# Performance work log

Hardware: AMD Instinct MI355X
Metric: run time of the kernel (lower is better)

## Reference

```python
import jax, jax.numpy as jnp
import numpy as np

B, T = 16, 2048
OBS_DIM, ACT_DIM, HIDDEN = 64, 16, 512


def setup_inputs() -> dict:
    key = jax.random.key(0)
    ks = jax.random.split(key, 6)
    n = lambda k, shape, scale: (jax.random.normal(k, shape, dtype=jnp.float32) * scale)
    return {
        "obs": n(ks[0], (B, T, OBS_DIM), 1.0),
        "act": n(ks[1], (B, T, ACT_DIM), 1.0),
        "W_e": n(ks[2], (HIDDEN, OBS_DIM + ACT_DIM), 0.05),   # embed Linear weight
        "b_e": jnp.zeros((HIDDEN,), jnp.float32),             # embed Linear bias
        "a_raw": n(ks[3], (HIDDEN,), 0.5),                    # diagonal decay (pre-tanh)
        "W_B": n(ks[4], (HIDDEN, HIDDEN), 0.02),              # B Linear weight (no bias)
        "W_out": n(ks[5], (OBS_DIM, HIDDEN), 0.04),           # out Linear weight
        "b_out": jnp.zeros((OBS_DIM,), jnp.float32),          # out Linear bias
    }


def reference(obs, act, W_e, b_e, a_raw, W_B, W_out, b_out):
    # x: [B, T, obs+act]
    x = jnp.concatenate([obs, act], axis=-1)
    # embed: Linear + ReLU, batched over all timesteps -> u: [B, T, H]
    u = jax.nn.relu(jnp.einsum('btd,hd->bth', x, W_e) + b_e)
    # B projection batched over all t (the per-step matmul in the torch loop)
    v = jnp.einsum('bth,gh->btg', u, W_B)  # [B, T, H]
    a = jnp.tanh(a_raw)  # [H]
    # Diagonal linear recurrence s_t = a * s_{t-1} + v_t, s_0 starting from zeros,
    # realized as a parallel (log-depth) associative scan over (decay, input) pairs.
    A = jnp.broadcast_to(a, v.shape)
    def combine(c1, c2):
        a1, b1 = c1
        a2, b2 = c2
        return (a1 * a2, a2 * b1 + b2)
    _, s = jax.lax.associative_scan(combine, (A, v), axis=1)  # s: [B, T, H]
    # out projection per step -> preds: [B, T, obs_dim]
    return jnp.einsum('bth,oh->bto', s, W_out) + b_out
```

## Files before the change

### kernel.cpp

```cpp
#include <hip/hip_runtime.h>
#include <hip/hip_bf16.h>

#define B_    16
#define T_    2048
#define H_    512
#define BT_   32768
#define DIN   80
#define DPAD  96
#define L_    64
#define C_    32
#define O_    64
#define NCHUNK (BT_ / L_)

typedef __attribute__((ext_vector_type(8))) short short8;
typedef __attribute__((ext_vector_type(4))) float f32x4;
typedef __attribute__((ext_vector_type(4))) float float4v;

__device__ __forceinline__ float bf2f(unsigned short u) {
  union { unsigned int i; float f; } x; x.i = ((unsigned int)u) << 16; return x.f;
}
__device__ __forceinline__ unsigned short f2bf(float f) {
  union { float f; unsigned int i; } x; x.f = f;
  unsigned int r = x.i + 0x7fffu + ((x.i >> 16) & 1u);
  return (unsigned short)(r >> 16);
}

template<int RELU, int BIAS, int CE>
__global__ __launch_bounds__(512) void gemm_fn(
    const unsigned short* __restrict__ A, const unsigned short* __restrict__ Bt,
    const float* __restrict__ bias, unsigned short* __restrict__ Cb,
    int K,
    const float* __restrict__ powa,
    float* __restrict__ e)
{
  constexpr int BM = 128, BN = 512, BK = 32;
  constexpr int A_BYTES = BM * BK * 2;
  constexpr int TOT = A_BYTES + BN * BK * 2;
  constexpr int ROUNDS = TOT / (512 * 16);
  __shared__ __align__(16) unsigned char ldsb[2 * TOT];

  const int tid  = threadIdx.x;
  const int lane = tid & 63;
  const int wid  = tid >> 6;
  const int wr   = wid >> 2;
  const int wc   = wid & 3;
  const int row0 = (int)blockIdx.x * BM;

  auto stage = [&](int k0, int buf) {
    #pragma unroll
    for (int r = 0; r < ROUNDS; ++r) {
      const int o = r * 8192 + tid * 16;
      const unsigned short* gsrc;
      if (o < A_BYTES) {
        const int idx = o >> 1;
        const int row = idx / BK, kk = idx % BK;
        gsrc = A + (size_t)(row0 + row) * K + (k0 + kk);
      } else {
        const int idx = (o - A_BYTES) >> 1;
        const int row = idx / BK, kk = idx % BK;
        gsrc = Bt + (size_t)row * K + (k0 + kk);
      }
      __builtin_amdgcn_global_load_lds(
          (const __attribute__((address_space(1))) void*)gsrc,
          (__attribute__((address_space(3))) void*)(ldsb + buf * TOT + o),
          16, 0, 0);
    }
  };

  f32x4 acc[4][8];
  #pragma unroll
  for (int m = 0; m < 4; ++m)
    #pragma unroll
    for (int n = 0; n < 8; ++n) acc[m][n] = f32x4{0.f, 0.f, 0.f, 0.f};

  const int NT = K / BK;
  stage(0, 0);
  __syncthreads();
  int cur = 0;
  for (int t = 0; t < NT; ++t) {
    if (t + 1 < NT) stage((t + 1) * BK, cur ^ 1);

    const unsigned short* base = (const unsigned short*)(ldsb + cur * TOT);
    const unsigned short* pA = base + (wr * 64 + (lane & 15)) * BK + ((lane >> 4) * 8);
    const unsigned short* pB = base + (A_BYTES / 2) + (wc * 128 + (lane & 15)) * BK + ((lane >> 4) * 8);
    short8 af[4];
    #pragma unroll
    for (int m = 0; m < 4; ++m) af[m] = *(const short8*)(pA + m * 16 * BK);
    #pragma unroll
    for (int n = 0; n < 8; ++n) {
      const short8 bfr = *(const short8*)(pB + n * 16 * BK);
      #pragma unroll
      for (int m = 0; m < 4; ++m)
        acc[m][n] = __builtin_amdgcn_mfma_f32_16x16x32_bf16(af[m], bfr, acc[m][n], 0, 0, 0);
    }

    __syncthreads();
    cur ^= 1;
  }

  const int cl = lane & 15, rg = (lane >> 4) * 4;
  #pragma unroll
  for (int m = 0; m < 4; ++m) {
    #pragma unroll
    for (int n = 0; n < 8; ++n) {
      #pragma unroll
      for (int e2 = 0; e2 < 4; ++e2) {
        const int gr = row0 + wr * 64 + m * 16 + rg + e2;
        const int gc = wc * 128 + n * 16 + cl;
        float v = acc[m][n][e2];
        if (BIAS) v += bias[gc];
        if (RELU) v = fmaxf(v, 0.f);
        Cb[(size_t)gr * BN + gc] = f2bf(v);
      }
    }
  }

  if (CE) {
    const int chunk = (row0 + wr * 64) >> 6;
    #pragma unroll
    for (int n = 0; n < 8; ++n) {
      const int h = wc * 128 + n * 16 + cl;
      const float a16 = powa[15 * H_ + h];
      float ep = 0.f;
      #pragma unroll
      for (int e2 = 0; e2 < 4; ++e2) {
        const int k = 15 - rg - e2;
        const float wk = (k == 0) ? 1.f : powa[(size_t)(k - 1) * H_ + h];
        float hsum = acc[0][n][e2];
        hsum = fmaf(hsum, a16, acc[1][n][e2]);
        hsum = fmaf(hsum, a16, acc[2][n][e2]);
        hsum = fmaf(hsum, a16, acc[3][n][e2]);
        ep = fmaf(wk, hsum, ep);
      }
      ep += __shfl_xor(ep, 16);
      ep += __shfl_xor(ep, 32);
      if ((lane >> 4) == 0)
        e[(size_t)chunk * H_ + h] = ep;
    }
  }
}

#define PX_N  (BT_ * 12)
#define WE_N  (H_ * DPAD)
#define WB_N  (H_ * H_)
#define WO_N  (O_ * H_)
#define PW_N  (WE_N + WB_N + WO_N + H_)
#define PREP_THREADS (PX_N + PW_N)

__global__ __launch_bounds__(256) void prep(
    const float* __restrict__ obs, const float* __restrict__ act,
    const float* __restrict__ W_e, const float* __restrict__ W_B,
    const float* __restrict__ W_out, const float* __restrict__ a_raw,
    unsigned short* __restrict__ xb,
    unsigned short* __restrict__ Web, unsigned short* __restrict__ WBb,
    unsigned short* __restrict__ Woutb, float* __restrict__ aarr,
    float* __restrict__ powa)
{
  const int gid = blockIdx.x * 256 + threadIdx.x;
  if (gid < PX_N) {
    const int g = gid % 12, n = gid / 12;
    float f[8];
    if (g < 8) {
      const float4v f0 = ((const float4v*)obs)[(size_t)n * 16 + g * 2];
      const float4v f1 = ((const float4v*)obs)[(size_t)n * 16 + g * 2 + 1];
      f[0]=f0[0]; f[1]=f0[1]; f[2]=f0[2]; f[3]=f0[3];
      f[4]=f1[0]; f[5]=f1[1]; f[6]=f1[2]; f[7]=f1[3];
    } else if (g < 10) {
      const float4v f0 = ((const float4v*)act)[(size_t)n * 4 + (g - 8) * 2];
      const float4v f1 = ((const float4v*)act)[(size_t)n * 4 + (g - 8) * 2 + 1];
      f[0]=f0[0]; f[1]=f0[1]; f[2]=f0[2]; f[3]=f0[3];
      f[4]=f1[0]; f[5]=f1[1]; f[6]=f1[2]; f[7]=f1[3];
    } else {
      #pragma unroll
      for (int i = 0; i < 8; ++i) f[i] = 0.f;
    }
    short8 o;
    #pragma unroll
    for (int i = 0; i < 8; ++i) o[i] = (short)f2bf(f[i]);
    *(short8*)(xb + (size_t)gid * 8) = o;
    return;
  }
  const int idx = gid - PX_N;
  if (idx < WE_N) {
    const int h = idx / DPAD, d = idx % DPAD;
    Web[idx] = f2bf(d < DIN ? W_e[h * DIN + d] : 0.f);
  } else if (idx < WE_N + WB_N) {
    const int j = idx - WE_N;
    WBb[j] = f2bf(W_B[j]);
  } else if (idx < WE_N + WB_N + WO_N) {
    const int j = idx - (WE_N + WB_N);
    Woutb[j] = f2bf(W_out[j]);
  } else if (idx < PW_N) {
    const int h = idx - (WE_N + WB_N + WO_N);
    const float a = tanhf(a_raw[h]);
    aarr[h] = a;
    float p = a;
    #pragma unroll
    for (int i = 0; i < 16; ++i) { powa[i * H_ + h] = p; p *= a; }
  }
}

__global__ __launch_bounds__(256) void scan_out(
    const unsigned int* __restrict__ v,
    const float* __restrict__ e,
    const float* __restrict__ aarr,
    const unsigned short* __restrict__ Wo,
    const float* __restrict__ b_out,
    float* __restrict__ y)
{
  __shared__ __align__(16) unsigned char sbytes[64 * 1024];
  const int blk = blockIdx.x;
  const int b = blk >> 5, c = blk & 31;
  const int tid = threadIdx.x;
  const int lane = tid & 63, w = tid >> 6;
  const int row_base = blk * L_;

  {
    const int h0 = tid * 2;
    const float a0 = aarr[h0], a1 = aarr[h0 + 1];
    float aL0 = a0 * a0, aL1 = a1 * a1;
    aL0 *= aL0; aL1 *= aL1;
    aL0 *= aL0; aL1 *= aL1;
    aL0 *= aL0; aL1 *= aL1;
    aL0 *= aL0; aL1 *= aL1;
    aL0 *= aL0; aL1 *= aL1;
    float s0 = 0.f, s1 = 0.f;
    for (int j = 0; j < c; ++j) {
      const size_t o = ((size_t)(b * C_ + j)) * H_ + h0;
      s0 = fmaf(aL0, s0, e[o]);
      s1 = fmaf(aL1, s1, e[o + 1]);
    }
    const unsigned int* vp = v + (size_t)row_base * (H_ / 2) + tid;
    #pragma unroll 8
    for (int t = 0; t < L_; ++t) {
      const unsigned int pv = vp[(size_t)t * (H_ / 2)];
      s0 = fmaf(a0, s0, bf2f((unsigned short)(pv & 0xffff)));
      s1 = fmaf(a1, s1, bf2f((unsigned short)(pv >> 16)));
      const int byte = t * 1024 + ((tid * 4) ^ ((t & 7) << 4));
      *(unsigned int*)(sbytes + byte) =
          (unsigned int)f2bf(s0) | ((unsigned int)f2bf(s1) << 16);
    }
  }
  __syncthreads();

  f32x4 acc[4];
  #pragma unroll
  for (int n = 0; n < 4; ++n) acc[n] = f32x4{0.f, 0.f, 0.f, 0.f};
  const int r = w * 16 + (lane & 15);
  const int kof = (lane >> 4) * 8;
  #pragma unroll 4
  for (int k0 = 0; k0 < H_; k0 += 32) {
    const int byte = r * 1024 + (((k0 + kof) * 2) ^ ((r & 7) << 4));
    const short8 af = *(const short8*)(sbytes + byte);
    #pragma unroll
    for (int n = 0; n < 4; ++n) {
      const short8 bf = *(const short8*)(Wo + (size_t)(n * 16 + (lane & 15)) * H_ + k0 + kof);
      acc[n] = __builtin_amdgcn_mfma_f32_16x16x32_bf16(af, bf, acc[n], 0, 0, 0);
    }
  }
  const int cl = lane & 15, rg = (lane >> 4) * 4;
  #pragma unroll
  for (int n = 0; n < 4; ++n) {
    #pragma unroll
    for (int e2 = 0; e2 < 4; ++e2) {
      const int gr = row_base + w * 16 + rg + e2;
      const int gc = n * 16 + cl;
      y[(size_t)gr * O_ + gc] = acc[n][e2] + b_out[gc];
    }
  }
}

extern "C" void kernel_launch(void* const* d_in, const int* in_sizes, int n_in,
                              void* d_out, int out_size, void* d_ws, size_t ws_size,
                              hipStream_t stream)
{
  const float* obs   = (const float*)d_in[0];
  const float* act   = (const float*)d_in[1];
  const float* W_e   = (const float*)d_in[2];
  const float* b_e   = (const float*)d_in[3];
  const float* a_raw = (const float*)d_in[4];
  const float* W_B   = (const float*)d_in[5];
  const float* W_out = (const float*)d_in[6];
  const float* b_out = (const float*)d_in[7];
  float* y = (float*)d_out;

  char* w = (char*)d_ws;
  auto carve = [&](size_t bytes) {
    char* p = w; w += (bytes + 255) & ~(size_t)255; return p;
  };
  unsigned short* xb    = (unsigned short*)carve((size_t)BT_ * DPAD * 2);
  unsigned short* Web   = (unsigned short*)carve((size_t)H_ * DPAD * 2);
  unsigned short* WBb   = (unsigned short*)carve((size_t)H_ * H_ * 2);
  unsigned short* Woutb = (unsigned short*)carve((size_t)O_ * H_ * 2);
  float*          aarr  = (float*)carve((size_t)H_ * 4);
  float*          powa  = (float*)carve((size_t)16 * H_ * 4);
  unsigned short* u     = (unsigned short*)carve((size_t)BT_ * H_ * 2);
  unsigned short* v     = (unsigned short*)carve((size_t)BT_ * H_ * 2);
  float*          e     = (float*)carve((size_t)NCHUNK * H_ * 4);

  prep<<<PREP_THREADS / 256, 256, 0, stream>>>(obs, act, W_e, W_B, W_out,
                                               a_raw, xb, Web, WBb, Woutb,
                                               aarr, powa);
  gemm_fn<1, 1, 0><<<BT_ / 128, 512, 0, stream>>>(
      xb, Web, b_e, u, DPAD, nullptr, nullptr);
  gemm_fn<0, 0, 1><<<BT_ / 128, 512, 0, stream>>>(
      u, WBb, nullptr, v, H_, powa, e);
  scan_out<<<NCHUNK, 256, 0, stream>>>((const unsigned int*)v, e, aarr,
                                       Woutb, b_out, y);
}
```

Baseline: 79.03 us.

## Fuse embed GEMM and B-projection GEMM keeping u tile in LDS

Merges the two GEMM launches into one kernel. Each block computes its 128-row embedded tile u, applies bias and ReLU, and writes it to LDS in an XOR-swizzled layout. It then runs the B projection from LDS, so the 32 MB u intermediate is never written to or read back from global memory. Weight fragments are now read straight from global/L2 instead of being staged through double-buffered LDS. That may add latency, and the 128 KB of LDS limits occupancy to one block per CU.

```diff
diff --git a/kernel.cpp b/kernel.cpp
--- a/kernel.cpp
+++ b/kernel.cpp
@@ -25,80 +25,107 @@
   return (unsigned short)(r >> 16);
 }
 
-template<int RELU, int BIAS, int CE>
-__global__ __launch_bounds__(512) void gemm_fn(
-    const unsigned short* __restrict__ A, const unsigned short* __restrict__ Bt,
-    const float* __restrict__ bias, unsigned short* __restrict__ Cb,
-    int K,
+__global__ __launch_bounds__(512) void embed_bproj(
+    const unsigned short* __restrict__ xb,
+    const unsigned short* __restrict__ Web,
+    const unsigned short* __restrict__ WBb,
+    const float* __restrict__ b_e,
     const float* __restrict__ powa,
+    unsigned short* __restrict__ v,
     float* __restrict__ e)
 {
-  constexpr int BM = 128, BN = 512, BK = 32;
-  constexpr int A_BYTES = BM * BK * 2;
-  constexpr int TOT = A_BYTES + BN * BK * 2;
-  constexpr int ROUNDS = TOT / (512 * 16);
-  __shared__ __align__(16) unsigned char ldsb[2 * TOT];
+  __shared__ __align__(16) unsigned char lds[128 * 1024];
 
   const int tid  = threadIdx.x;
   const int lane = tid & 63;
   const int wid  = tid >> 6;
   const int wr   = wid >> 2;
   const int wc   = wid & 3;
-  const int row0 = (int)blockIdx.x * BM;
-
-  auto stage = [&](int k0, int buf) {
-    #pragma unroll
-    for (int r = 0; r < ROUNDS; ++r) {
-      const int o = r * 8192 + tid * 16;
-      const unsigned short* gsrc;
-      if (o < A_BYTES) {
-        const int idx = o >> 1;
-        const int row = idx / BK, kk = idx % BK;
-        gsrc = A + (size_t)(row0 + row) * K + (k0 + kk);
-      } else {
-        const int idx = (o - A_BYTES) >> 1;
-        const int row = idx / BK, kk = idx % BK;
-        gsrc = Bt + (size_t)row * K + (k0 + kk);
+  const int row0 = (int)blockIdx.x * 128;
+  const int cl   = lane & 15;
+  const int kgrp = lane >> 4;
+  const int rg   = kgrp * 4;
+
+  #pragma unroll
+  for (int r = 0; r < 3; ++r) {
+    const int o = r * 8192 + tid * 16;
+    const int idx = o >> 1;
+    const int row = idx / DPAD, kk = idx % DPAD;
+    __builtin_amdgcn_global_load_lds(
+        (const __attribute__((address_space(1))) void*)
+            (xb + (size_t)(row0 + row) * DPAD + kk),
+        (__attribute__((address_space(3))) void*)(lds + o), 16, 0, 0);
+  }
+  __syncthreads();
+
+  f32x4 acc[4][8];
+  #pragma unroll
+  for (int m = 0; m < 4; ++m)
+    #pragma unroll
+    for (int n = 0; n < 8; ++n) acc[m][n] = f32x4{0.f, 0.f, 0.f, 0.f};
+
+  #pragma unroll
+  for (int t = 0; t < 3; ++t) {
+    const int k0 = t * 32;
+    short8 af[4];
+    #pragma unroll
+    for (int m = 0; m < 4; ++m)
+      af[m] = *(const short8*)(lds + (wr * 64 + m * 16 + cl) * (DPAD * 2)
+                                   + (k0 + kgrp * 8) * 2);
+    #pragma unroll
+    for (int n = 0; n < 8; ++n) {
+      const int col = wc * 128 + n * 16 + cl;
+      const short8 bf = *(const short8*)(Web + (size_t)col * DPAD + k0 + kgrp * 8);
+      #pragma unroll
+      for (int m = 0; m < 4; ++m)
+        acc[m][n] = __builtin_amdgcn_mfma_f32_16x16x32_bf16(af[m], bf, acc[m][n], 0, 0, 0);
+    }
+  }
+  __syncthreads();
+
+  #pragma unroll
+  for (int n = 0; n < 8; ++n) {
+    const int col = wc * 128 + n * 16 + cl;
+    const float be = b_e[col];
+    const int cb = col * 2;
+    #pragma unroll
+    for (int m = 0; m < 4; ++m) {
+      #pragma unroll
+      for (int e2 = 0; e2 < 4; ++e2) {
+        const int row = wr * 64 + m * 16 + rg + e2;
+        const float uu = fmaxf(acc[m][n][e2] + be, 0.f);
+        const int byte = row * 1024 + (cb & 15) + ((((cb >> 4) ^ (row & 7))) << 4);
+        *(unsigned short*)(lds + byte) = f2bf(uu);
       }
-      __builtin_amdgcn_global_load_lds(
-          (const __attribute__((address_space(1))) void*)gsrc,
-          (__attribute__((address_space(3))) void*)(ldsb + buf * TOT + o),
-          16, 0, 0);
-    }
-  };
-
-  f32x4 acc[4][8];
+    }
+  }
+  __syncthreads();
+
   #pragma unroll
   for (int m = 0; m < 4; ++m)
     #pragma unroll
     for (int n = 0; n < 8; ++n) acc[m][n] = f32x4{0.f, 0.f, 0.f, 0.f};
 
-  const int NT = K / BK;
-  stage(0, 0);
-  __syncthreads();
-  int cur = 0;
-  for (int t = 0; t < NT; ++t) {
-    if (t + 1 < NT) stage((t + 1) * BK, cur ^ 1);
-
-    const unsigned short* base = (const unsigned short*)(ldsb + cur * TOT);
-    const unsigned short* pA = base + (wr * 64 + (lane & 15)) * BK + ((lane >> 4) * 8);
-    const unsigned short* pB = base + (A_BYTES / 2) + (wc * 128 + (lane & 15)) * BK + ((lane >> 4) * 8);
+  #pragma unroll 2
+  for (int t = 0; t < 16; ++t) {
+    const int k0 = t * 32;
+    const int kb = (k0 + kgrp * 8) * 2;
     short8 af[4];
     #pragma unroll
-    for (int m = 0; m < 4; ++m) af[m] = *(const short8*)(pA + m * 16 * BK);
+    for (int m = 0; m < 4; ++m) {
+      const int row = wr * 64 + m * 16 + cl;
+      af[m] = *(const short8*)(lds + row * 1024 + (((kb >> 4) ^ (row & 7)) << 4));
+    }
     #pragma unroll
     for (int n = 0; n < 8; ++n) {
-      const short8 bfr = *(const short8*)(pB + n * 16 * BK);
+      const int col = wc * 128 + n * 16 + cl;
+      const short8 bf = *(const short8*)(WBb + (size_t)col * H_ + k0 + kgrp * 8);
       #pragma unroll
       for (int m = 0; m < 4; ++m)
-        acc[m][n] = __builtin_amdgcn_mfma_f32_16x16x32_bf16(af[m], bfr, acc[m][n], 0, 0, 0);
-    }
-
-    __syncthreads();
-    cur ^= 1;
-  }
-
-  const int cl = lane & 15, rg = (lane >> 4) * 4;
+        acc[m][n] = __builtin_amdgcn_mfma_f32_16x16x32_bf16(af[m], bf, acc[m][n], 0, 0, 0);
+    }
+  }
+
   #pragma unroll
   for (int m = 0; m < 4; ++m) {
     #pragma unroll
@@ -107,15 +134,12 @@
       for (int e2 = 0; e2 < 4; ++e2) {
         const int gr = row0 + wr * 64 + m * 16 + rg + e2;
         const int gc = wc * 128 + n * 16 + cl;
-        float v = acc[m][n][e2];
-        if (BIAS) v += bias[gc];
-        if (RELU) v = fmaxf(v, 0.f);
-        Cb[(size_t)gr * BN + gc] = f2bf(v);
+        v[(size_t)gr * H_ + gc] = f2bf(acc[m][n][e2]);
       }
     }
   }
 
-  if (CE) {
+  {
     const int chunk = (row0 + wr * 64) >> 6;
     #pragma unroll
     for (int n = 0; n < 8; ++n) {
@@ -294,17 +318,13 @@
   unsigned short* Woutb = (unsigned short*)carve((size_t)O_ * H_ * 2);
   float*          aarr  = (float*)carve((size_t)H_ * 4);
   float*          powa  = (float*)carve((size_t)16 * H_ * 4);
-  unsigned short* u     = (unsigned short*)carve((size_t)BT_ * H_ * 2);
   unsigned short* v     = (unsigned short*)carve((size_t)BT_ * H_ * 2);
   float*          e     = (float*)carve((size_t)NCHUNK * H_ * 4);
 
   prep<<<PREP_THREADS / 256, 256, 0, stream>>>(obs, act, W_e, W_B, W_out,
                                                a_raw, xb, Web, WBb, Woutb,
                                                aarr, powa);
-  gemm_fn<1, 1, 0><<<BT_ / 128, 512, 0, stream>>>(
-      xb, Web, b_e, u, DPAD, nullptr, nullptr);
-  gemm_fn<0, 0, 1><<<BT_ / 128, 512, 0, stream>>>(
-      u, WBb, nullptr, v, H_, powa, e);
+  embed_bproj<<<BT_ / 128, 512, 0, stream>>>(xb, Web, WBb, b_e, powa, v, e);
   scan_out<<<NCHUNK, 256, 0, stream>>>((const unsigned int*)v, e, aarr,
                                        Woutb, b_out, y);
 }
```

After: 85.61 us. 1.08x slower.

## Rewrite GEMMs with 256x256 tiles, XOR-swizzled LDS and staggered A/B prefetch

Applied to the files above, without the earlier changes.

Replaces the 128x512 tile GEMM (BK=32) with a 256x256 tile kernel using BK=64, an XOR-swizzled LDS layout to avoid bank conflicts, and a pipeline that prefetches B two steps ahead and A one step ahead with explicit waitcnt and barriers. It also remaps blocks with an XCD-aware index. To make the embed GEMM fit BK=64 it pads the input dim from 96 to 128, which adds zero work. The aim is better operand reuse and MFMA utilisation, at the cost of 128KB of LDS per block and only 256 blocks.

```diff
diff --git a/kernel.cpp b/kernel.cpp
--- a/kernel.cpp
+++ b/kernel.cpp
@@ -6,7 +6,7 @@
 #define H_    512
 #define BT_   32768
 #define DIN   80
-#define DPAD  96
+#define DPAD  128
 #define L_    64
 #define C_    32
 #define O_    64
@@ -25,122 +25,169 @@
   return (unsigned short)(r >> 16);
 }
 
-template<int RELU, int BIAS, int CE>
-__global__ __launch_bounds__(512) void gemm_fn(
+template<int NT, int RELU, int BIAS, int CE>
+__global__ __launch_bounds__(512) void gemm256(
     const unsigned short* __restrict__ A, const unsigned short* __restrict__ Bt,
     const float* __restrict__ bias, unsigned short* __restrict__ Cb,
-    int K,
+    int ldk,
     const float* __restrict__ powa,
     float* __restrict__ e)
 {
-  constexpr int BM = 128, BN = 512, BK = 32;
-  constexpr int A_BYTES = BM * BK * 2;
-  constexpr int TOT = A_BYTES + BN * BK * 2;
-  constexpr int ROUNDS = TOT / (512 * 16);
-  __shared__ __align__(16) unsigned char ldsb[2 * TOT];
+  __shared__ __align__(16) unsigned char lds[131072];
 
   const int tid  = threadIdx.x;
   const int lane = tid & 63;
   const int wid  = tid >> 6;
   const int wr   = wid >> 2;
   const int wc   = wid & 3;
-  const int row0 = (int)blockIdx.x * BM;
-
-  auto stage = [&](int k0, int buf) {
-    #pragma unroll
-    for (int r = 0; r < ROUNDS; ++r) {
-      const int o = r * 8192 + tid * 16;
-      const unsigned short* gsrc;
-      if (o < A_BYTES) {
-        const int idx = o >> 1;
-        const int row = idx / BK, kk = idx % BK;
-        gsrc = A + (size_t)(row0 + row) * K + (k0 + kk);
-      } else {
-        const int idx = (o - A_BYTES) >> 1;
-        const int row = idx / BK, kk = idx % BK;
-        gsrc = Bt + (size_t)row * K + (k0 + kk);
+  const int cl   = lane & 15;
+  const int kgrp = lane >> 4;
+  const int rg   = kgrp * 4;
+
+  const int X  = (int)blockIdx.x & 7;
+  const int j  = (int)blockIdx.x >> 3;
+  const int mt = X * 16 + (j >> 1);
+  const int nt = j & 1;
+  const int row0 = mt * 256, col0 = nt * 256;
+
+  auto stageA = [&](int q, int buf) {
+    const int k0 = q * 64;
+    #pragma unroll
+    for (int r = 0; r < 4; ++r) {
+      const int o   = r * 8192 + tid * 16;
+      const int row = o >> 7;
+      const int c16 = (o >> 4) & 7;
+      const int kk  = (c16 ^ (row & 7)) << 3;
+      __builtin_amdgcn_global_load_lds(
+          (const __attribute__((address_space(1))) void*)
+              (A + (size_t)(row0 + row) * ldk + k0 + kk),
+          (__attribute__((address_space(3))) void*)(lds + buf * 65536 + o),
+          16, 0, 0);
+    }
+  };
+  auto stageB = [&](int q, int buf) {
+    const int k0 = q * 64;
+    #pragma unroll
+    for (int r = 0; r < 4; ++r) {
+      const int o   = r * 8192 + tid * 16;
+      const int col = o >> 7;
+      const int c16 = (o >> 4) & 7;
+      const int kk  = (c16 ^ (col & 7)) << 3;
+      __builtin_amdgcn_global_load_lds(
+          (const __attribute__((address_space(1))) void*)
+              (Bt + (size_t)(col0 + col) * ldk + k0 + kk),
+          (__attribute__((address_space(3))) void*)(lds + buf * 65536 + 32768 + o),
+          16, 0, 0);
+    }
+  };
+
+  f32x4 acc[8][4];
+  #pragma unroll
+  for (int m = 0; m < 8; ++m)
+    #pragma unroll
+    for (int n = 0; n < 4; ++n) acc[m][n] = f32x4{0.f, 0.f, 0.f, 0.f};
+
+  stageA(0, 0); stageB(0, 0); stageB(1, 1);
+  asm volatile("s_waitcnt vmcnt(4)" ::: "memory");
+  __builtin_amdgcn_sched_barrier(0);
+  __builtin_amdgcn_s_barrier();
+
+  for (int q = 0; q < NT; ++q) {
+    const int cur = q & 1;
+    const unsigned char* bufp = lds + cur * 65536;
+
+    if (q + 1 < NT) stageA(q + 1, cur ^ 1);
+
+    short8 bfr[4][2];
+    #pragma unroll
+    for (int n = 0; n < 4; ++n) {
+      const int col = wc * 64 + n * 16 + cl;
+      #pragma unroll
+      for (int ks = 0; ks < 2; ++ks)
+        bfr[n][ks] = *(const short8*)(bufp + 32768 + col * 128 +
+                                      ((((ks << 2) + kgrp) ^ (col & 7)) << 4));
+    }
+    asm volatile("s_waitcnt lgkmcnt(0)" ::: "memory");
+    __builtin_amdgcn_sched_barrier(0);
+    __builtin_amdgcn_s_barrier();
+
+    if (q + 2 < NT) stageB(q + 2, cur);
+
+    #pragma unroll
+    for (int g = 0; g < 4; ++g) {
+      short8 af[2][2];
+      #pragma unroll
+      for (int mm = 0; mm < 2; ++mm) {
+        const int row = wr * 128 + (g * 2 + mm) * 16 + cl;
+        #pragma unroll
+        for (int ks = 0; ks < 2; ++ks)
+          af[mm][ks] = *(const short8*)(bufp + row * 128 +
+                                        ((((ks << 2) + kgrp) ^ (row & 7)) << 4));
       }
-      __builtin_amdgcn_global_load_lds(
-          (const __attribute__((address_space(1))) void*)gsrc,
-          (__attribute__((address_space(3))) void*)(ldsb + buf * TOT + o),
-          16, 0, 0);
-    }
-  };
-
-  f32x4 acc[4][8];
+      #pragma unroll
+      for (int ks = 0; ks < 2; ++ks)
+        #pragma unroll
+        for (int mm = 0; mm < 2; ++mm)
+          #pragma unroll
+          for (int n = 0; n < 4; ++n)
+            acc[g * 2 + mm][n] = __builtin_amdgcn_mfma_f32_16x16x32_bf16(
+                af[mm][ks], bfr[n][ks], acc[g * 2 + mm][n], 0, 0, 0);
+    }
+
+    if (q + 2 < NT) {
+      asm volatile("s_waitcnt vmcnt(4)" ::: "memory");
+    } else if (q + 1 < NT) {
+      asm volatile("s_waitcnt vmcnt(0)" ::: "memory");
+    }
+    __builtin_amdgcn_sched_barrier(0);
+    __builtin_amdgcn_s_barrier();
+  }
+
   #pragma unroll
-  for (int m = 0; m < 4; ++m)
-    #pragma unroll
-    for (int n = 0; n < 8; ++n) acc[m][n] = f32x4{0.f, 0.f, 0.f, 0.f};
-
-  const int NT = K / BK;
-  stage(0, 0);
-  __syncthreads();
-  int cur = 0;
-  for (int t = 0; t < NT; ++t) {
-    if (t + 1 < NT) stage((t + 1) * BK, cur ^ 1);
-
-    const unsigned short* base = (const unsigned short*)(ldsb + cur * TOT);
-    const unsigned short* pA = base + (wr * 64 + (lane & 15)) * BK + ((lane >> 4) * 8);
-    const unsigned short* pB = base + (A_BYTES / 2) + (wc * 128 + (lane & 15)) * BK + ((lane >> 4) * 8);
-    short8 af[4];
-    #pragma unroll
-    for (int m = 0; m < 4; ++m) af[m] = *(const short8*)(pA + m * 16 * BK);
-    #pragma unroll
-    for (int n = 0; n < 8; ++n) {
-      const short8 bfr = *(const short8*)(pB + n * 16 * BK);
-      #pragma unroll
-      for (int m = 0; m < 4; ++m)
-        acc[m][n] = __builtin_amdgcn_mfma_f32_16x16x32_bf16(af[m], bfr, acc[m][n], 0, 0, 0);
-    }
-
-    __syncthreads();
-    cur ^= 1;
-  }
-
-  const int cl = lane & 15, rg = (lane >> 4) * 4;
-  #pragma unroll
-  for (int m = 0; m < 4; ++m) {
-    #pragma unroll
-    for (int n = 0; n < 8; ++n) {
+  for (int m = 0; m < 8; ++m) {
+    #pragma unroll
+    for (int n = 0; n < 4; ++n) {
+      const int gc = col0 + wc * 64 + n * 16 + cl;
       #pragma unroll
       for (int e2 = 0; e2 < 4; ++e2) {
-        const int gr = row0 + wr * 64 + m * 16 + rg + e2;
-        const int gc = wc * 128 + n * 16 + cl;
+        const int gr = row0 + wr * 128 + m * 16 + rg + e2;
         float v = acc[m][n][e2];
         if (BIAS) v += bias[gc];
         if (RELU) v = fmaxf(v, 0.f);
-        Cb[(size_t)gr * BN + gc] = f2bf(v);
+        Cb[(size_t)gr * H_ + gc] = f2bf(v);
       }
     }
   }
 
   if (CE) {
-    const int chunk = (row0 + wr * 64) >> 6;
-    #pragma unroll
-    for (int n = 0; n < 8; ++n) {
-      const int h = wc * 128 + n * 16 + cl;
-      const float a16 = powa[15 * H_ + h];
-      float ep = 0.f;
-      #pragma unroll
-      for (int e2 = 0; e2 < 4; ++e2) {
-        const int k = 15 - rg - e2;
-        const float wk = (k == 0) ? 1.f : powa[(size_t)(k - 1) * H_ + h];
-        float hsum = acc[0][n][e2];
-        hsum = fmaf(hsum, a16, acc[1][n][e2]);
-        hsum = fmaf(hsum, a16, acc[2][n][e2]);
-        hsum = fmaf(hsum, a16, acc[3][n][e2]);
-        ep = fmaf(wk, hsum, ep);
+    #pragma unroll
+    for (int c = 0; c < 2; ++c) {
+      const int chunk = ((row0 + wr * 128) >> 6) + c;
+      #pragma unroll
+      for (int n = 0; n < 4; ++n) {
+        const int h = col0 + wc * 64 + n * 16 + cl;
+        const float a16 = powa[15 * H_ + h];
+        float ep = 0.f;
+        #pragma unroll
+        for (int e2 = 0; e2 < 4; ++e2) {
+          const int k = 15 - rg - e2;
+          const float wk = (k == 0) ? 1.f : powa[(size_t)(k - 1) * H_ + h];
+          float hsum = acc[c * 4 + 0][n][e2];
+          hsum = fmaf(hsum, a16, acc[c * 4 + 1][n][e2]);
+          hsum = fmaf(hsum, a16, acc[c * 4 + 2][n][e2]);
+          hsum = fmaf(hsum, a16, acc[c * 4 + 3][n][e2]);
+          ep = fmaf(wk, hsum, ep);
+        }
+        ep += __shfl_xor(ep, 16);
+        ep += __shfl_xor(ep, 32);
+        if (kgrp == 0)
+          e[(size_t)chunk * H_ + h] = ep;
       }
-      ep += __shfl_xor(ep, 16);
-      ep += __shfl_xor(ep, 32);
-      if ((lane >> 4) == 0)
-        e[(size_t)chunk * H_ + h] = ep;
-    }
-  }
-}
-
-#define PX_N  (BT_ * 12)
+    }
+  }
+}
+
+#define PX_N  (BT_ * 16)
 #define WE_N  (H_ * DPAD)
 #define WB_N  (H_ * H_)
 #define WO_N  (O_ * H_)
@@ -158,7 +205,7 @@
 {
   const int gid = blockIdx.x * 256 + threadIdx.x;
   if (gid < PX_N) {
-    const int g = gid % 12, n = gid / 12;
+    const int g = gid & 15, n = gid >> 4;
     float f[8];
     if (g < 8) {
       const float4v f0 = ((const float4v*)obs)[(size_t)n * 16 + g * 2];
@@ -182,7 +229,7 @@
   }
   const int idx = gid - PX_N;
   if (idx < WE_N) {
-    const int h = idx / DPAD, d = idx % DPAD;
+    const int h = idx >> 7, d = idx & 127;
     Web[idx] = f2bf(d < DIN ? W_e[h * DIN + d] : 0.f);
   } else if (idx < WE_N + WB_N) {
     const int j = idx - WE_N;
@@ -301,9 +348,9 @@
   prep<<<PREP_THREADS / 256, 256, 0, stream>>>(obs, act, W_e, W_B, W_out,
                                                a_raw, xb, Web, WBb, Woutb,
                                                aarr, powa);
-  gemm_fn<1, 1, 0><<<BT_ / 128, 512, 0, stream>>>(
+  gemm256<2, 1, 1, 0><<<256, 512, 0, stream>>>(
       xb, Web, b_e, u, DPAD, nullptr, nullptr);
-  gemm_fn<0, 0, 1><<<BT_ / 128, 512, 0, stream>>>(
+  gemm256<8, 0, 0, 1><<<256, 512, 0, stream>>>(
       u, WBb, nullptr, v, H_, powa, e);
   scan_out<<<NCHUNK, 256, 0, stream>>>((const unsigned int*)v, e, aarr,
                                        Woutb, b_out, y);
```

New measurement: 75.52 us. 1.05x faster.
